# Performance work log

Measured on AMD Instinct MI355X. Metric: run time of the kernel, lower is better.

The kernel has to match this reference:

```python
import math
import jax, jax.numpy as jnp
import numpy as np

B, C, H, W = 32, 256, 32, 32  # in==mid==out channels

def setup_inputs() -> dict:
    key = jax.random.key(0)
    ks = jax.random.split(key, 3)
    x = jax.random.normal(ks[0], (B, C, H, W), dtype=jnp.float32)
    # 1x1 convs are just channel matmuls: weight [out_ch, in_ch]
    w_in = jax.random.normal(ks[1], (3 * C, C), dtype=jnp.float32) * (1.0 / math.sqrt(C))
    b_in = jnp.zeros((3 * C,), dtype=jnp.float32)
    # project_out has init_scale=0.0 in the original; we use random weights so the
    # output (and gradients) are non-trivial, but the math is identical.
    w_out = jax.random.normal(ks[2], (C, C), dtype=jnp.float32) * (1.0 / math.sqrt(C))
    b_out = jnp.zeros((C,), dtype=jnp.float32)
    return {"x": x, "w_in": w_in, "b_in": b_in, "w_out": w_out, "b_out": b_out}

def _qkv_attention(q, k, v):
    # q,k,v: [B,C,H,W]. Full spatial self-attention over the HxW grid.
    b, c, h, w = q.shape
    scores = jnp.einsum('bchw,bcHW->bhwHW', q, k)          # [B,H,W,H,W]
    scores = scores.reshape(b, h, w, h * w) / math.sqrt(c)
    attn = jax.nn.softmax(scores, axis=-1).reshape(b, h, w, h, w)
    return jnp.einsum('bhwHW,bcHW->bchw', attn, v)          # [B,C,H,W]

def reference(x, w_in, b_in, w_out, b_out):
    skip = x  # in_channels == out_channels -> Identity skip
    qkv = jnp.einsum('oc,bchw->bohw', w_in, x) + b_in[None, :, None, None]
    q, k, v = jnp.split(qkv, 3, axis=1)
    h = _qkv_attention(q, k, v)
    out = jnp.einsum('oc,bchw->bohw', w_out, h) + b_out[None, :, None, None]
    return out + skip
```

## Files before the change

### kernel.cpp

```cpp
#include <hip/hip_runtime.h>
#include <hip/hip_bf16.h>

typedef __attribute__((ext_vector_type(8))) short bf16x8;
typedef __attribute__((ext_vector_type(4))) float f32x4;
typedef __attribute__((ext_vector_type(16))) float f32x16;
typedef long long i64;

#define NB 32
#define NC 256
#define NN 1024

__device__ __forceinline__ unsigned pack2(float a, float b) {
    __hip_bfloat16 ha = __float2bfloat16(a), hb = __float2bfloat16(b);
    unsigned short ua = *(unsigned short*)&ha, ub = *(unsigned short*)&hb;
    return (unsigned)ua | ((unsigned)ub << 16);
}

__device__ __forceinline__ float bflo(unsigned u) {
    union { unsigned i; float f; } x; x.i = u << 16; return x.f;
}
__device__ __forceinline__ float bfhi(unsigned u) {
    union { unsigned i; float f; } x; x.i = u & 0xffff0000u; return x.f;
}
__device__ __forceinline__ unsigned fp8x4(float a, float b, float c, float d) {
    int w = __builtin_amdgcn_cvt_pk_fp8_f32(a, b, 0, false);
    w = __builtin_amdgcn_cvt_pk_fp8_f32(c, d, w, true);
    return (unsigned)w;
}

__device__ __forceinline__ void glds16(const void* g, void* lds) {
    __builtin_amdgcn_global_load_lds(
        (const __attribute__((address_space(1))) unsigned int*)g,
        (__attribute__((address_space(3))) unsigned int*)lds, 16, 0, 0);
}

__global__ __launch_bounds__(256) void xpose_kernel(
    const float* __restrict__ x, unsigned char* __restrict__ Xt8)
{
    __shared__ float Ls[64 * 67];
    const int t = threadIdx.x;
    const int n0 = blockIdx.x * 64, c0 = blockIdx.y * 64, b = blockIdx.z;
    const int cl = t >> 4, nl = (t & 15) * 4;
    const float* xb = x + ((size_t)b * NC + c0) * NN + n0;
    #pragma unroll
    for (int q4 = 0; q4 < 4; ++q4) {
        const int c = cl + q4 * 16;
        const float4 v = *(const float4*)(xb + (size_t)c * NN + nl);
        Ls[(nl + 0) * 67 + c] = v.x;
        Ls[(nl + 1) * 67 + c] = v.y;
        Ls[(nl + 2) * 67 + c] = v.z;
        Ls[(nl + 3) * 67 + c] = v.w;
    }
    __syncthreads();
    #pragma unroll
    for (int p = 0; p < 2; ++p) {
        const int idx = p * 256 + t, n = idx >> 3, cs = idx & 7;
        const float* r = &Ls[n * 67 + cs * 8];
        uint2 o;
        o.x = fp8x4(r[0], r[1], r[2], r[3]);
        o.y = fp8x4(r[4], r[5], r[6], r[7]);
        *(uint2*)(Xt8 + ((size_t)b * NN + n0 + n) * 256 + c0 + cs * 8) = o;
    }
}

__device__ __forceinline__ void stage_ab8(const unsigned char* __restrict__ Ag,
                                          const float* __restrict__ Bg,
                                          char* Ad, char* Bd, int ks, int t)
{
    #pragma unroll
    for (int p = 0; p < 2; ++p) {
        const int idx = p * 256 + t;
        const int row = idx >> 2, pc = idx & 3;
        const int lp = pc ^ (row & 3);
        glds16(Ag + (size_t)row * 256 + ks * 64 + lp * 16, Ad + idx * 16);
        const float* wp = Bg + (size_t)row * NC + ks * 64 + lp * 16;
        const float4 u0 = *(const float4*)wp;
        const float4 u1 = *(const float4*)(wp + 4);
        const float4 u2 = *(const float4*)(wp + 8);
        const float4 u3 = *(const float4*)(wp + 12);
        uint4 pk;
        pk.x = fp8x4(u0.x, u0.y, u0.z, u0.w);
        pk.y = fp8x4(u1.x, u1.y, u1.z, u1.w);
        pk.z = fp8x4(u2.x, u2.y, u2.z, u2.w);
        pk.w = fp8x4(u3.x, u3.y, u3.z, u3.w);
        *(uint4*)(Bd + idx * 16) = pk;
    }
}

__global__ __launch_bounds__(256, 3) void qkv_gemm_kernel(
    const unsigned char* __restrict__ Xt8, const float* __restrict__ w_in,
    const float* __restrict__ b_in, unsigned char* __restrict__ Qt8,
    unsigned char* __restrict__ Kt8, unsigned char* __restrict__ Vf8)
{
    __shared__ char smem[34816];
    char* const A0 = smem;
    char* const A1 = smem + 8192;
    char* const B0 = smem + 16384;
    char* const B1 = smem + 24576;

    const int t  = threadIdx.x;
    const int wv = t >> 6, ln = t & 63, lo = ln & 15, hi = ln >> 4;
    const int wm = wv >> 1, wn = wv & 1;
    const int n0 = blockIdx.x * 128, o0 = blockIdx.y * 128, b = blockIdx.z;

    const unsigned char* Ag = Xt8 + ((size_t)b * NN + n0) * 256;
    const float* Bg = w_in + (size_t)o0 * NC;

    f32x4 acc[4][4];
    #pragma unroll
    for (int i = 0; i < 4; ++i)
        #pragma unroll
        for (int j = 0; j < 4; ++j) acc[i][j] = (f32x4){0.f, 0.f, 0.f, 0.f};

    int ra[4], rb[4];
    #pragma unroll
    for (int f = 0; f < 4; ++f) { ra[f] = wm * 64 + f * 16 + lo; rb[f] = wn * 64 + f * 16 + lo; }

    stage_ab8(Ag, Bg, A0, B0, 0, t);
    __syncthreads();
    #pragma unroll
    for (int ks = 0; ks < 4; ++ks) {
        char* Ac = (ks & 1) ? A1 : A0;
        char* Bc = (ks & 1) ? B1 : B0;
        if (ks < 3)
            stage_ab8(Ag, Bg, (ks & 1) ? A0 : A1, (ks & 1) ? B0 : B1, ks + 1, t);
        #pragma unroll
        for (int kk = 0; kk < 2; ++kk) {
            i64 av[4], bv[4];
            #pragma unroll
            for (int f = 0; f < 4; ++f) {
                av[f] = *(const i64*)(Ac + ra[f] * 64 + (((kk << 2) | hi) ^ ((ra[f] & 3) << 1)) * 8);
                bv[f] = *(const i64*)(Bc + rb[f] * 64 + (((kk << 2) | hi) ^ ((rb[f] & 3) << 1)) * 8);
            }
            #pragma unroll
            for (int fm = 0; fm < 4; ++fm)
                #pragma unroll
                for (int fn = 0; fn < 4; ++fn)
                    acc[fm][fn] = __builtin_amdgcn_mfma_f32_16x16x32_fp8_fp8(
                        av[fm], bv[fn], acc[fm][fn], 0, 0, 0);
        }
        __syncthreads();
    }

    float bias[4];
    #pragma unroll
    for (int fn = 0; fn < 4; ++fn) bias[fn] = b_in[o0 + wn * 64 + fn * 16 + lo];

    __hip_bfloat16* Ls = (__hip_bfloat16*)smem;
    if (o0 < 512) {
        #pragma unroll
        for (int fm = 0; fm < 4; ++fm)
            #pragma unroll
            for (int fn = 0; fn < 4; ++fn)
                #pragma unroll
                for (int r = 0; r < 4; ++r)
                    Ls[(wm * 64 + fm * 16 + hi * 4 + r) * 136 + wn * 64 + fn * 16 + lo] =
                        __float2bfloat16(acc[fm][fn][r] + bias[fn]);
        __syncthreads();
        unsigned char* dst = (o0 < 256) ? Qt8 : Kt8;
        const int oc = (o0 < 256) ? o0 : o0 - 256;
        #pragma unroll
        for (int p = 0; p < 4; ++p) {
            const int idx = p * 256 + t, row = idx >> 3, ch = idx & 7;
            const unsigned* ls = (const unsigned*)&Ls[row * 136 + ch * 16];
            const uint4 a = *(const uint4*)ls;
            const uint4 b2 = *(const uint4*)(ls + 4);
            uint4 o;
            o.x = fp8x4(bflo(a.x), bfhi(a.x), bflo(a.y), bfhi(a.y));
            o.y = fp8x4(bflo(a.z), bfhi(a.z), bflo(a.w), bfhi(a.w));
            o.z = fp8x4(bflo(b2.x), bfhi(b2.x), bflo(b2.y), bfhi(b2.y));
            o.w = fp8x4(bflo(b2.z), bfhi(b2.z), bflo(b2.w), bfhi(b2.w));
            *(uint4*)(dst + ((size_t)b * NN + n0 + row) * 256 + oc + ch * 16) = o;
        }
    } else {
        #pragma unroll
        for (int fm = 0; fm < 4; ++fm)
            #pragma unroll
            for (int fn = 0; fn < 4; ++fn)
                #pragma unroll
                for (int r = 0; r < 4; ++r)
                    Ls[(wn * 64 + fn * 16 + lo) * 136 + wm * 64 + fm * 16 + hi * 4 + r] =
                        __float2bfloat16(acc[fm][fn][r] + bias[fn]);
        __syncthreads();
        #pragma unroll
        for (int p = 0; p < 8; ++p) {
            const int idx = p * 256 + t;
            const int ch = idx >> 7, cr = idx & 127;
            const unsigned* ls = (const unsigned*)&Ls[cr * 136 + ch * 8];
            const uint4 a = *(const uint4*)ls;
            uint2 o;
            o.x = fp8x4(bflo(a.x), bfhi(a.x), bflo(a.y), bfhi(a.y));
            o.y = fp8x4(bflo(a.z), bfhi(a.z), bflo(a.w), bfhi(a.w));
            const int g = (n0 >> 3) + ch;
            *(uint2*)(Vf8 + (((size_t)b * 128 + g) * 256 + (o0 - 512) + cr) * 8) = o;
        }
    }
}

__device__ __forceinline__ void stage_tile(const unsigned char* __restrict__ Kb,
                                           const unsigned char* __restrict__ Vb,
                                           char* Kd, char* Vd, int m0, int t)
{
    {
        const int row = t >> 4, pc = t & 15;
        const int prow = (row & 19) | ((row & 4) << 1) | ((row & 8) >> 1);
        const int sc = pc ^ (row & 15);
        glds16(Kb + (size_t)(m0 + prow) * 256 + sc * 16, Kd + t * 16);
    }
    {
        glds16(Vb + (size_t)(m0 >> 3) * 2048 + t * 16, Vd + t * 16);
    }
}

__global__ __launch_bounds__(512, 2) void attn_kernel(
    const unsigned char* __restrict__ Qt8, const unsigned char* __restrict__ Kt8,
    const unsigned char* __restrict__ Vf8, const float* __restrict__ w_out,
    const float* __restrict__ b_out, const float* __restrict__ xg,
    float* __restrict__ out)
{
    __shared__ char smem[139264];

    const int t  = threadIdx.x;
    const int wv = t >> 6, ln = t & 63;
    const int l32 = ln & 31, h2 = ln >> 5;
    const int qgrp = wv & 3, half = wv >> 2;
    const int wid = blockIdx.x + 8 * blockIdx.y;
    const int swz = (wid & 7) * 32 + (wid >> 3);
    const int qb = swz & 7, b = swz >> 3;
    const int n0 = qb * 128;
    const float scale = 0.0625f;

    const unsigned char* Kbase = Kt8 + (size_t)b * NN * 256;
    const unsigned char* Vbase = Vf8 + (size_t)b * 128 * 2048;

    const unsigned char* qp = Qt8 + ((size_t)b * NN + n0 + qgrp * 32 + l32) * 256;
    i64 qf[16];
    #pragma unroll
    for (int ks = 0; ks < 16; ++ks)
        qf[ks] = *(const i64*)(qp + ks * 16 + h2 * 8);

    f32x16 acc[8];
    #pragma unroll
    for (int ct = 0; ct < 8; ++ct)
        #pragma unroll
        for (int r = 0; r < 16; ++r) acc[ct][r] = 0.f;
    float mr = 0.f;
    float sr = 0.f;

    #pragma unroll
    for (int tt = 0; tt < 4; ++tt)
        stage_tile(Kbase, Vbase, smem + tt * 8192, smem + 32768 + tt * 8192,
                   tt * 32, t);
    __syncthreads();

    for (int s = 0; s < 16; ++s) {
        if (s < 15) {
            const int t2 = 2 * s + 2, t3 = 2 * s + 3;
            stage_tile(Kbase, Vbase, smem + (t2 & 3) * 8192,
                       smem + 32768 + (t2 & 3) * 8192, t2 * 32, t);
            stage_tile(Kbase, Vbase, smem + (t3 & 3) * 8192,
                       smem + 32768 + (t3 & 3) * 8192, t3 * 32, t);
        }
        const int tile = 2 * s + half;
        char* const Kc = smem + (tile & 3) * 8192;
        char* const Vc = smem + 32768 + (tile & 3) * 8192;

        f32x16 sfA, sfB;
        #pragma unroll
        for (int r = 0; r < 16; ++r) { sfA[r] = 0.f; sfB[r] = 0.f; }
        __builtin_amdgcn_s_setprio(1);
        #pragma unroll
        for (int ks = 0; ks < 8; ++ks) {
            const int pc = ks ^ (l32 & 15);
            const i64 kf = *(const i64*)(Kc + l32 * 256 + pc * 16 + h2 * 8);
            sfA = __builtin_amdgcn_mfma_f32_32x32x16_fp8_fp8(kf, qf[ks], sfA, 0, 0, 0);
        }
        #pragma unroll
        for (int ks = 8; ks < 16; ++ks) {
            const int pc = ks ^ (l32 & 15);
            const i64 kf = *(const i64*)(Kc + l32 * 256 + pc * 16 + h2 * 8);
            sfB = __builtin_amdgcn_mfma_f32_32x32x16_fp8_fp8(kf, qf[ks], sfB, 0, 0, 0);
        }
        __builtin_amdgcn_s_setprio(0);

        float sv[16];
        #pragma unroll
        for (int r = 0; r < 16; ++r) sv[r] = sfA[r] + sfB[r];

        float m0a = fmaxf(sv[0], sv[1]),  m1a = fmaxf(sv[2], sv[3]);
        float m2a = fmaxf(sv[4], sv[5]),  m3a = fmaxf(sv[6], sv[7]);
        float m4a = fmaxf(sv[8], sv[9]),  m5a = fmaxf(sv[10], sv[11]);
        float m6a = fmaxf(sv[12], sv[13]), m7a = fmaxf(sv[14], sv[15]);
        float m0b = fmaxf(m0a, m1a), m1b = fmaxf(m2a, m3a);
        float m2b = fmaxf(m4a, m5a), m3b = fmaxf(m6a, m7a);
        float tm = fmaxf(fmaxf(m0b, m1b), fmaxf(m2b, m3b));
        tm = fmaxf(tm, __shfl_xor(tm, 32, 64));
        tm *= scale;
        if (__any(tm > mr + 8.f)) {
            const float mn = fmaxf(mr, tm);
            const float al = __expf(mr - mn);
            mr = mn;
            sr *= al;
            #pragma unroll
            for (int ct = 0; ct < 8; ++ct)
                #pragma unroll
                for (int r = 0; r < 16; ++r) acc[ct][r] *= al;
        }
        float p[16];
        #pragma unroll
        for (int r = 0; r < 16; ++r)
            p[r] = __expf(sv[r] * scale - mr);
        float s0a = p[0] + p[1],  s1a = p[2] + p[3];
        float s2a = p[4] + p[5],  s3a = p[6] + p[7];
        float s4a = p[8] + p[9],  s5a = p[10] + p[11];
        float s6a = p[12] + p[13], s7a = p[14] + p[15];
        float sacc = ((s0a + s1a) + (s2a + s3a)) + ((s4a + s5a) + (s6a + s7a));
        sacc += __shfl_xor(sacc, 32, 64);
        sr += sacc;

        i64 pb[2];
        #pragma unroll
        for (int kstep = 0; kstep < 2; ++kstep) {
            union { unsigned u[2]; i64 l; } uu;
            uu.u[0] = fp8x4(p[8 * kstep + 0], p[8 * kstep + 1],
                            p[8 * kstep + 2], p[8 * kstep + 3]);
            uu.u[1] = fp8x4(p[8 * kstep + 4], p[8 * kstep + 5],
                            p[8 * kstep + 6], p[8 * kstep + 7]);
            pb[kstep] = uu.l;
        }

        __builtin_amdgcn_s_setprio(1);
        #pragma unroll
        for (int ct = 0; ct < 8; ++ct) {
            #pragma unroll
            for (int kstep = 0; kstep < 2; ++kstep) {
                const i64 vf = *(const i64*)(Vc + (2 * kstep + h2) * 2048 +
                                             (ct * 32 + l32) * 8);
                acc[ct] = __builtin_amdgcn_mfma_f32_32x32x16_fp8_fp8(vf, pb[kstep], acc[ct], 0, 0, 0);
            }
        }
        __builtin_amdgcn_s_setprio(0);
        __syncthreads();
    }

    const int wo = t >> 5, wck = t & 31;
    float4 wr[16];
    #pragma unroll
    for (int p = 0; p < 8; ++p) {
        const int o = p * 16 + wo;
        const float* wp = w_out + (size_t)o * NC + wck * 8;
        wr[2 * p]     = *(const float4*)wp;
        wr[2 * p + 1] = *(const float4*)(wp + 4);
    }

    float* const ex = (float*)smem;
    __hip_bfloat16* const Hld = (__hip_bfloat16*)(smem + 69632);
    #pragma unroll
    for (int ph = 0; ph < 2; ++ph) {
        if (half == 1 && (qgrp >> 1) == ph) {
            float* dst = ex + ((qgrp & 1) * 64 + ln) * 132;
            #pragma unroll
            for (int ct = 0; ct < 8; ++ct)
                #pragma unroll
                for (int rr = 0; rr < 4; ++rr) {
                    f32x4 v = {acc[ct][rr * 4 + 0], acc[ct][rr * 4 + 1],
                               acc[ct][rr * 4 + 2], acc[ct][rr * 4 + 3]};
                    *(f32x4*)(dst + ct * 16 + rr * 4) = v;
                }
            dst[128] = mr;
            dst[129] = sr;
        }
        __syncthreads();
        if (half == 0 && (qgrp >> 1) == ph) {
            const float* src = ex + ((qgrp & 1) * 64 + ln) * 132;
            const float mb = src[128], lb = src[129];
            const float m = fmaxf(mr, mb);
            float fa = __expf(mr - m), fb = __expf(mb - m);
            const float inv = 1.0f / (sr * fa + lb * fb);
            fa *= inv; fb *= inv;
            __hip_bfloat16* hrow = Hld + (size_t)(qgrp * 32 + l32) * 264;
            #pragma unroll
            for (int ct = 0; ct < 8; ++ct)
                #pragma unroll
                for (int ss = 0; ss < 4; ++ss) {
                    const float o0 = acc[ct][ss * 4 + 0] * fa + src[ct * 16 + ss * 4 + 0] * fb;
                    const float o1 = acc[ct][ss * 4 + 1] * fa + src[ct * 16 + ss * 4 + 1] * fb;
                    const float o2 = acc[ct][ss * 4 + 2] * fa + src[ct * 16 + ss * 4 + 2] * fb;
                    const float o3 = acc[ct][ss * 4 + 3] * fa + src[ct * 16 + ss * 4 + 3] * fb;
                    uint2 v;
                    v.x = pack2(o0, o1);
                    v.y = pack2(o2, o3);
                    *(uint2*)(hrow + ct * 32 + ss * 8 + h2 * 4) = v;
                }
        }
        __syncthreads();
    }

    __hip_bfloat16* const Wld = (__hip_bfloat16*)smem;
    const int oT = wv >> 1;
    const int nT0 = (wv & 1) * 2, nT1 = nT0 + 1;

    #pragma unroll
    for (int p = 0; p < 8; ++p) {
        const int o = p * 16 + wo;
        uint4 pk;
        pk.x = pack2(wr[2*p].x, wr[2*p].y);     pk.y = pack2(wr[2*p].z, wr[2*p].w);
        pk.z = pack2(wr[2*p+1].x, wr[2*p+1].y); pk.w = pack2(wr[2*p+1].z, wr[2*p+1].w);
        *(uint4*)((char*)Wld + (size_t)o * 528 + wck * 16) = pk;
    }
    #pragma unroll
    for (int p = 0; p < 8; ++p) {
        const int o = 128 + p * 16 + wo;
        const float* wp = w_out + (size_t)o * NC + wck * 8;
        wr[2 * p]     = *(const float4*)wp;
        wr[2 * p + 1] = *(const float4*)(wp + 4);
    }
    __syncthreads();

    #pragma unroll
    for (int oh = 0; oh < 2; ++oh) {
        f32x16 oc0, oc1;
        #pragma unroll
        for (int r = 0; r < 16; ++r) { oc0[r] = 0.f; oc1[r] = 0.f; }
        __builtin_amdgcn_s_setprio(1);
        #pragma unroll
        for (int ks = 0; ks < 16; ++ks) {
            const int ck = ks * 2 + h2;
            bf16x8 wf = *(const bf16x8*)((char*)Wld + (size_t)(oT * 32 + l32) * 528 + ck * 16);
            bf16x8 hf0 = *(const bf16x8*)((char*)Hld + (size_t)(nT0 * 32 + l32) * 528 + ck * 16);
            bf16x8 hf1 = *(const bf16x8*)((char*)Hld + (size_t)(nT1 * 32 + l32) * 528 + ck * 16);
            oc0 = __builtin_amdgcn_mfma_f32_32x32x16_bf16(wf, hf0, oc0, 0, 0, 0);
            oc1 = __builtin_amdgcn_mfma_f32_32x32x16_bf16(wf, hf1, oc1, 0, 0, 0);
        }
        __builtin_amdgcn_s_setprio(0);

        #pragma unroll
        for (int r = 0; r < 16; ++r) {
            const int o = oh * 128 + oT * 32 + (r & 3) + 8 * (r >> 2) + 4 * h2;
            const float bo = b_out[o];
            const size_t rowg = ((size_t)b * NC + o) * NN + n0;
            const size_t g0 = rowg + nT0 * 32 + l32;
            const size_t g1 = rowg + nT1 * 32 + l32;
            out[g0] = oc0[r] + bo + xg[g0];
            out[g1] = oc1[r] + bo + xg[g1];
        }
        __syncthreads();
        if (oh == 0) {
            #pragma unroll
            for (int p = 0; p < 8; ++p) {
                const int o = p * 16 + wo;
                uint4 pk;
                pk.x = pack2(wr[2*p].x, wr[2*p].y);     pk.y = pack2(wr[2*p].z, wr[2*p].w);
                pk.z = pack2(wr[2*p+1].x, wr[2*p+1].y); pk.w = pack2(wr[2*p+1].z, wr[2*p+1].w);
                *(uint4*)((char*)Wld + (size_t)o * 528 + wck * 16) = pk;
            }
            __syncthreads();
        }
    }
}

extern "C" void kernel_launch(void* const* d_in, const int* in_sizes, int n_in,
                              void* d_out, int out_size, void* d_ws, size_t ws_size,
                              hipStream_t stream) {
    const float* x     = (const float*)d_in[0];
    const float* w_in  = (const float*)d_in[1];
    const float* b_in  = (const float*)d_in[2];
    const float* w_out = (const float*)d_in[3];
    const float* b_out = (const float*)d_in[4];
    float* out = (float*)d_out;

    if (ws_size < (size_t)64 * 1024 * 1024) return;
    char* ws = (char*)d_ws;
    unsigned char* Qt8 = (unsigned char*)(ws);
    unsigned char* Kt8 = (unsigned char*)(ws + ((size_t)8 << 20));
    unsigned char* Vf8 = (unsigned char*)(ws + ((size_t)16 << 20));
    unsigned char* Xt8 = (unsigned char*)(ws + ((size_t)24 << 20));

    xpose_kernel<<<dim3(16, 4, 32), 256, 0, stream>>>(x, Xt8);
    qkv_gemm_kernel<<<dim3(8, 6, 32), 256, 0, stream>>>(Xt8, w_in, b_in, Qt8, Kt8, Vf8);
    attn_kernel<<<dim3(8, 32), 512, 0, stream>>>(Qt8, Kt8, Vf8, w_out, b_out, x, out);
}
```

Before: 84.37 us.

## Fuse input transpose and FP8 cast into the QKV GEMM, two output tiles per block

Drops the separate transpose kernel and the Xt8 intermediate. The QKV GEMM now streams fp32 x tiles straight into LDS with global_load_lds and builds the fp8 A-fragments in registers. Each block computes two output-channel tiles, so the x tile it loads serves both. This saves one launch and a global round-trip of x, but adds LDS gathers and fp8 conversion inside the GEMM loop, more accumulator registers, and lower occupancy (launch bound 2, larger LDS).

```diff
diff --git a/kernel.cpp b/kernel.cpp
--- a/kernel.cpp
+++ b/kernel.cpp
@@ -34,167 +34,163 @@
         (__attribute__((address_space(3))) unsigned int*)lds, 16, 0, 0);
 }
 
-__global__ __launch_bounds__(256) void xpose_kernel(
-    const float* __restrict__ x, unsigned char* __restrict__ Xt8)
-{
-    __shared__ float Ls[64 * 67];
-    const int t = threadIdx.x;
-    const int n0 = blockIdx.x * 64, c0 = blockIdx.y * 64, b = blockIdx.z;
-    const int cl = t >> 4, nl = (t & 15) * 4;
-    const float* xb = x + ((size_t)b * NC + c0) * NN + n0;
-    #pragma unroll
-    for (int q4 = 0; q4 < 4; ++q4) {
-        const int c = cl + q4 * 16;
-        const float4 v = *(const float4*)(xb + (size_t)c * NN + nl);
-        Ls[(nl + 0) * 67 + c] = v.x;
-        Ls[(nl + 1) * 67 + c] = v.y;
-        Ls[(nl + 2) * 67 + c] = v.z;
-        Ls[(nl + 3) * 67 + c] = v.w;
-    }
-    __syncthreads();
-    #pragma unroll
-    for (int p = 0; p < 2; ++p) {
-        const int idx = p * 256 + t, n = idx >> 3, cs = idx & 7;
-        const float* r = &Ls[n * 67 + cs * 8];
-        uint2 o;
-        o.x = fp8x4(r[0], r[1], r[2], r[3]);
-        o.y = fp8x4(r[4], r[5], r[6], r[7]);
-        *(uint2*)(Xt8 + ((size_t)b * NN + n0 + n) * 256 + c0 + cs * 8) = o;
-    }
-}
-
-__device__ __forceinline__ void stage_ab8(const unsigned char* __restrict__ Ag,
-                                          const float* __restrict__ Bg,
-                                          char* Ad, char* Bd, int ks, int t)
-{
-    #pragma unroll
-    for (int p = 0; p < 2; ++p) {
-        const int idx = p * 256 + t;
-        const int row = idx >> 2, pc = idx & 3;
-        const int lp = pc ^ (row & 3);
-        glds16(Ag + (size_t)row * 256 + ks * 64 + lp * 16, Ad + idx * 16);
-        const float* wp = Bg + (size_t)row * NC + ks * 64 + lp * 16;
-        const float4 u0 = *(const float4*)wp;
-        const float4 u1 = *(const float4*)(wp + 4);
-        const float4 u2 = *(const float4*)(wp + 8);
-        const float4 u3 = *(const float4*)(wp + 12);
-        uint4 pk;
-        pk.x = fp8x4(u0.x, u0.y, u0.z, u0.w);
-        pk.y = fp8x4(u1.x, u1.y, u1.z, u1.w);
-        pk.z = fp8x4(u2.x, u2.y, u2.z, u2.w);
-        pk.w = fp8x4(u3.x, u3.y, u3.z, u3.w);
-        *(uint4*)(Bd + idx * 16) = pk;
-    }
-}
-
-__global__ __launch_bounds__(256, 3) void qkv_gemm_kernel(
-    const unsigned char* __restrict__ Xt8, const float* __restrict__ w_in,
+__global__ __launch_bounds__(256, 2) void qkv_fused_kernel(
+    const float* __restrict__ x, const float* __restrict__ w_in,
     const float* __restrict__ b_in, unsigned char* __restrict__ Qt8,
     unsigned char* __restrict__ Kt8, unsigned char* __restrict__ Vf8)
 {
-    __shared__ char smem[34816];
-    char* const A0 = smem;
-    char* const A1 = smem + 8192;
-    char* const B0 = smem + 16384;
-    char* const B1 = smem + 24576;
-
+    __shared__ char smem[49664];
     const int t  = threadIdx.x;
     const int wv = t >> 6, ln = t & 63, lo = ln & 15, hi = ln >> 4;
     const int wm = wv >> 1, wn = wv & 1;
-    const int n0 = blockIdx.x * 128, o0 = blockIdx.y * 128, b = blockIdx.z;
-
-    const unsigned char* Ag = Xt8 + ((size_t)b * NN + n0) * 256;
-    const float* Bg = w_in + (size_t)o0 * NC;
-
-    f32x4 acc[4][4];
-    #pragma unroll
-    for (int i = 0; i < 4; ++i)
-        #pragma unroll
-        for (int j = 0; j < 4; ++j) acc[i][j] = (f32x4){0.f, 0.f, 0.f, 0.f};
+    const int n0 = blockIdx.x * 128, y = blockIdx.y, b = blockIdx.z;
+    const int ot0 = y, ot1 = y + 3;
+
+    const float* xb = x + (size_t)b * NC * NN;
+
+    f32x4 acc[2][4][4];
+    #pragma unroll
+    for (int g = 0; g < 2; ++g)
+        #pragma unroll
+        for (int i = 0; i < 4; ++i)
+            #pragma unroll
+            for (int j = 0; j < 4; ++j) acc[g][i][j] = (f32x4){0.f, 0.f, 0.f, 0.f};
 
     int ra[4], rb[4];
     #pragma unroll
     for (int f = 0; f < 4; ++f) { ra[f] = wm * 64 + f * 16 + lo; rb[f] = wn * 64 + f * 16 + lo; }
 
-    stage_ab8(Ag, Bg, A0, B0, 0, t);
+    #define XBUF(bf) (smem + (bf) * 16640)
+    #define BBUF(bf, og) (smem + 33280 + (bf) * 8192 + (og) * 4096)
+    auto stage = [&](int ks, int bf) {
+        #pragma unroll
+        for (int p = 0; p < 4; ++p) {
+            const int idx = p * 256 + t;
+            const int pair = idx >> 6, sub = idx & 63;
+            const int c = ks * 32 + pair * 2 + (sub >> 5);
+            glds16(xb + (size_t)c * NN + n0 + (sub & 31) * 4, XBUF(bf) + pair * 1040);
+        }
+        #pragma unroll
+        for (int og = 0; og < 2; ++og) {
+            const int o = t >> 1, m = t & 1;
+            const int otile = og ? ot1 : ot0;
+            const float* wp = w_in + (size_t)(otile * 128 + o) * NC + ks * 32 + m * 16;
+            const float4 u0 = *(const float4*)wp;
+            const float4 u1 = *(const float4*)(wp + 4);
+            const float4 u2 = *(const float4*)(wp + 8);
+            const float4 u3 = *(const float4*)(wp + 12);
+            uint4 pk;
+            pk.x = fp8x4(u0.x, u0.y, u0.z, u0.w);
+            pk.y = fp8x4(u1.x, u1.y, u1.z, u1.w);
+            pk.z = fp8x4(u2.x, u2.y, u2.z, u2.w);
+            pk.w = fp8x4(u3.x, u3.y, u3.z, u3.w);
+            const int slot = m ^ ((o >> 2) & 1);
+            *(uint4*)(BBUF(bf, og) + o * 32 + slot * 16) = pk;
+        }
+    };
+
+    stage(0, 0);
     __syncthreads();
-    #pragma unroll
-    for (int ks = 0; ks < 4; ++ks) {
-        char* Ac = (ks & 1) ? A1 : A0;
-        char* Bc = (ks & 1) ? B1 : B0;
-        if (ks < 3)
-            stage_ab8(Ag, Bg, (ks & 1) ? A0 : A1, (ks & 1) ? B0 : B1, ks + 1, t);
-        #pragma unroll
-        for (int kk = 0; kk < 2; ++kk) {
-            i64 av[4], bv[4];
+    for (int ks = 0; ks < 8; ++ks) {
+        const int cur = ks & 1;
+        if (ks < 7) stage(ks + 1, cur ^ 1);
+
+        const float* Xc = (const float*)XBUF(cur);
+        i64 av[4];
+        #pragma unroll
+        for (int f = 0; f < 4; ++f) {
+            const int n = ra[f];
+            float v[8];
+            #pragma unroll
+            for (int j = 0; j < 8; ++j) {
+                const int c = hi * 8 + j;
+                v[j] = Xc[c * 128 + (c >> 1) * 4 + n];
+            }
+            union { unsigned u[2]; i64 l; } uu;
+            uu.u[0] = fp8x4(v[0], v[1], v[2], v[3]);
+            uu.u[1] = fp8x4(v[4], v[5], v[6], v[7]);
+            av[f] = uu.l;
+        }
+        #pragma unroll
+        for (int og = 0; og < 2; ++og) {
+            i64 bv[4];
             #pragma unroll
             for (int f = 0; f < 4; ++f) {
-                av[f] = *(const i64*)(Ac + ra[f] * 64 + (((kk << 2) | hi) ^ ((ra[f] & 3) << 1)) * 8);
-                bv[f] = *(const i64*)(Bc + rb[f] * 64 + (((kk << 2) | hi) ^ ((rb[f] & 3) << 1)) * 8);
+                const int o = rb[f];
+                const int phys8 = hi ^ (((o >> 2) & 1) << 1);
+                bv[f] = *(const i64*)(BBUF(cur, og) + o * 32 + phys8 * 8);
             }
             #pragma unroll
             for (int fm = 0; fm < 4; ++fm)
                 #pragma unroll
                 for (int fn = 0; fn < 4; ++fn)
-                    acc[fm][fn] = __builtin_amdgcn_mfma_f32_16x16x32_fp8_fp8(
-                        av[fm], bv[fn], acc[fm][fn], 0, 0, 0);
-        }
-        __syncthreads();
-    }
-
-    float bias[4];
-    #pragma unroll
-    for (int fn = 0; fn < 4; ++fn) bias[fn] = b_in[o0 + wn * 64 + fn * 16 + lo];
+                    acc[og][fm][fn] = __builtin_amdgcn_mfma_f32_16x16x32_fp8_fp8(
+                        av[fm], bv[fn], acc[og][fm][fn], 0, 0, 0);
+        }
+        __syncthreads();
+    }
 
     __hip_bfloat16* Ls = (__hip_bfloat16*)smem;
-    if (o0 < 512) {
-        #pragma unroll
-        for (int fm = 0; fm < 4; ++fm)
-            #pragma unroll
-            for (int fn = 0; fn < 4; ++fn)
-                #pragma unroll
-                for (int r = 0; r < 4; ++r)
-                    Ls[(wm * 64 + fm * 16 + hi * 4 + r) * 136 + wn * 64 + fn * 16 + lo] =
-                        __float2bfloat16(acc[fm][fn][r] + bias[fn]);
-        __syncthreads();
-        unsigned char* dst = (o0 < 256) ? Qt8 : Kt8;
-        const int oc = (o0 < 256) ? o0 : o0 - 256;
-        #pragma unroll
-        for (int p = 0; p < 4; ++p) {
-            const int idx = p * 256 + t, row = idx >> 3, ch = idx & 7;
-            const unsigned* ls = (const unsigned*)&Ls[row * 136 + ch * 16];
-            const uint4 a = *(const uint4*)ls;
-            const uint4 b2 = *(const uint4*)(ls + 4);
-            uint4 o;
-            o.x = fp8x4(bflo(a.x), bfhi(a.x), bflo(a.y), bfhi(a.y));
-            o.y = fp8x4(bflo(a.z), bfhi(a.z), bflo(a.w), bfhi(a.w));
-            o.z = fp8x4(bflo(b2.x), bfhi(b2.x), bflo(b2.y), bfhi(b2.y));
-            o.w = fp8x4(bflo(b2.z), bfhi(b2.z), bflo(b2.w), bfhi(b2.w));
-            *(uint4*)(dst + ((size_t)b * NN + n0 + row) * 256 + oc + ch * 16) = o;
-        }
-    } else {
-        #pragma unroll
-        for (int fm = 0; fm < 4; ++fm)
-            #pragma unroll
-            for (int fn = 0; fn < 4; ++fn)
-                #pragma unroll
-                for (int r = 0; r < 4; ++r)
-                    Ls[(wn * 64 + fn * 16 + lo) * 136 + wm * 64 + fm * 16 + hi * 4 + r] =
-                        __float2bfloat16(acc[fm][fn][r] + bias[fn]);
-        __syncthreads();
-        #pragma unroll
-        for (int p = 0; p < 8; ++p) {
-            const int idx = p * 256 + t;
-            const int ch = idx >> 7, cr = idx & 127;
-            const unsigned* ls = (const unsigned*)&Ls[cr * 136 + ch * 8];
-            const uint4 a = *(const uint4*)ls;
-            uint2 o;
-            o.x = fp8x4(bflo(a.x), bfhi(a.x), bflo(a.y), bfhi(a.y));
-            o.y = fp8x4(bflo(a.z), bfhi(a.z), bflo(a.w), bfhi(a.w));
-            const int g = (n0 >> 3) + ch;
-            *(uint2*)(Vf8 + (((size_t)b * 128 + g) * 256 + (o0 - 512) + cr) * 8) = o;
-        }
-    }
+    #pragma unroll
+    for (int og = 0; og < 2; ++og) {
+        const int otile = og ? ot1 : ot0;
+        const int o0 = otile * 128;
+        float bias[4];
+        #pragma unroll
+        for (int fn = 0; fn < 4; ++fn) bias[fn] = b_in[o0 + wn * 64 + fn * 16 + lo];
+
+        if (o0 < 512) {
+            #pragma unroll
+            for (int fm = 0; fm < 4; ++fm)
+                #pragma unroll
+                for (int fn = 0; fn < 4; ++fn)
+                    #pragma unroll
+                    for (int r = 0; r < 4; ++r)
+                        Ls[(wm * 64 + fm * 16 + hi * 4 + r) * 136 + wn * 64 + fn * 16 + lo] =
+                            __float2bfloat16(acc[og][fm][fn][r] + bias[fn]);
+            __syncthreads();
+            unsigned char* dst = (o0 < 256) ? Qt8 : Kt8;
+            const int oc = (o0 < 256) ? o0 : o0 - 256;
+            #pragma unroll
+            for (int p = 0; p < 4; ++p) {
+                const int idx = p * 256 + t, row = idx >> 3, ch = idx & 7;
+                const unsigned* ls = (const unsigned*)&Ls[row * 136 + ch * 16];
+                const uint4 a = *(const uint4*)ls;
+                const uint4 b2 = *(const uint4*)(ls + 4);
+                uint4 o;
+                o.x = fp8x4(bflo(a.x), bfhi(a.x), bflo(a.y), bfhi(a.y));
+                o.y = fp8x4(bflo(a.z), bfhi(a.z), bflo(a.w), bfhi(a.w));
+                o.z = fp8x4(bflo(b2.x), bfhi(b2.x), bflo(b2.y), bfhi(b2.y));
+                o.w = fp8x4(bflo(b2.z), bfhi(b2.z), bflo(b2.w), bfhi(b2.w));
+                *(uint4*)(dst + ((size_t)b * NN + n0 + row) * 256 + oc + ch * 16) = o;
+            }
+        } else {
+            #pragma unroll
+            for (int fm = 0; fm < 4; ++fm)
+                #pragma unroll
+                for (int fn = 0; fn < 4; ++fn)
+                    #pragma unroll
+                    for (int r = 0; r < 4; ++r)
+                        Ls[(wn * 64 + fn * 16 + lo) * 136 + wm * 64 + fm * 16 + hi * 4 + r] =
+                            __float2bfloat16(acc[og][fm][fn][r] + bias[fn]);
+            __syncthreads();
+            #pragma unroll
+            for (int p = 0; p < 8; ++p) {
+                const int idx = p * 256 + t;
+                const int ch = idx >> 7, cr = idx & 127;
+                const unsigned* ls = (const unsigned*)&Ls[cr * 136 + ch * 8];
+                const uint4 a = *(const uint4*)ls;
+                uint2 o;
+                o.x = fp8x4(bflo(a.x), bfhi(a.x), bflo(a.y), bfhi(a.y));
+                o.y = fp8x4(bflo(a.z), bfhi(a.z), bflo(a.w), bfhi(a.w));
+                const int g = (n0 >> 3) + ch;
+                *(uint2*)(Vf8 + (((size_t)b * 128 + g) * 256 + (o0 - 512) + cr) * 8) = o;
+            }
+        }
+        __syncthreads();
+    }
+    #undef XBUF
+    #undef BBUF
 }
 
 __device__ __forceinline__ void stage_tile(const unsigned char* __restrict__ Kb,
@@ -469,14 +465,12 @@
     const float* b_out = (const float*)d_in[4];
     float* out = (float*)d_out;
 
-    if (ws_size < (size_t)64 * 1024 * 1024) return;
+    if (ws_size < (size_t)24 * 1024 * 1024) return;
     char* ws = (char*)d_ws;
     unsigned char* Qt8 = (unsigned char*)(ws);
     unsigned char* Kt8 = (unsigned char*)(ws + ((size_t)8 << 20));
     unsigned char* Vf8 = (unsigned char*)(ws + ((size_t)16 << 20));
-    unsigned char* Xt8 = (unsigned char*)(ws + ((size_t)24 << 20));
-
-    xpose_kernel<<<dim3(16, 4, 32), 256, 0, stream>>>(x, Xt8);
-    qkv_gemm_kernel<<<dim3(8, 6, 32), 256, 0, stream>>>(Xt8, w_in, b_in, Qt8, Kt8, Vf8);
+
+    qkv_fused_kernel<<<dim3(8, 3, 32), 256, 0, stream>>>(x, w_in, b_in, Qt8, Kt8, Vf8);
     attn_kernel<<<dim3(8, 32), 512, 0, stream>>>(Qt8, Kt8, Vf8, w_out, b_out, x, out);
 }
```

Result: slower. 87.39 us (+3.6%).

## Software-pipeline PV MFMAs one tile behind QK MFMAs in attention loop

Applied to the files above, without the earlier changes.

Defers each tile's P·V MFMA accumulation to the next loop iteration, where it is issued right after the current tile's QK^T MFMAs. The aim is to overlap the softmax/exp work with matrix work and shorten the per-iteration dependency chain. To keep the deferred V tile alive, V staging grows from 4 to 8 LDS slots, and a tail PV step runs after the loop. The w_out prefetch into registers is replaced by a direct load-convert-store per output half, which lowers register pressure but adds a global load before each projection half.

```diff
diff --git a/kernel.cpp b/kernel.cpp
--- a/kernel.cpp
+++ b/kernel.cpp
@@ -249,21 +249,25 @@
 
     #pragma unroll
     for (int tt = 0; tt < 4; ++tt)
-        stage_tile(Kbase, Vbase, smem + tt * 8192, smem + 32768 + tt * 8192,
-                   tt * 32, t);
+        stage_tile(Kbase, Vbase, smem + (tt & 3) * 8192,
+                   smem + 32768 + (tt & 7) * 8192, tt * 32, t);
     __syncthreads();
+
+    i64 pb_prev[2];
+    pb_prev[0] = 0; pb_prev[1] = 0;
+    const char* Vc_prev = smem + 32768;
 
     for (int s = 0; s < 16; ++s) {
         if (s < 15) {
             const int t2 = 2 * s + 2, t3 = 2 * s + 3;
             stage_tile(Kbase, Vbase, smem + (t2 & 3) * 8192,
-                       smem + 32768 + (t2 & 3) * 8192, t2 * 32, t);
+                       smem + 32768 + (t2 & 7) * 8192, t2 * 32, t);
             stage_tile(Kbase, Vbase, smem + (t3 & 3) * 8192,
-                       smem + 32768 + (t3 & 3) * 8192, t3 * 32, t);
+                       smem + 32768 + (t3 & 7) * 8192, t3 * 32, t);
         }
         const int tile = 2 * s + half;
         char* const Kc = smem + (tile & 3) * 8192;
-        char* const Vc = smem + 32768 + (tile & 3) * 8192;
+        char* const Vc = smem + 32768 + (tile & 7) * 8192;
 
         f32x16 sfA, sfB;
         #pragma unroll
@@ -280,6 +284,18 @@
             const int pc = ks ^ (l32 & 15);
             const i64 kf = *(const i64*)(Kc + l32 * 256 + pc * 16 + h2 * 8);
             sfB = __builtin_amdgcn_mfma_f32_32x32x16_fp8_fp8(kf, qf[ks], sfB, 0, 0, 0);
+        }
+
+        if (s > 0) {
+            #pragma unroll
+            for (int ct = 0; ct < 8; ++ct) {
+                #pragma unroll
+                for (int kstep = 0; kstep < 2; ++kstep) {
+                    const i64 vf = *(const i64*)(Vc_prev + (2 * kstep + h2) * 2048 +
+                                                 (ct * 32 + l32) * 8);
+                    acc[ct] = __builtin_amdgcn_mfma_f32_32x32x16_fp8_fp8(vf, pb_prev[kstep], acc[ct], 0, 0, 0);
+                }
+            }
         }
         __builtin_amdgcn_s_setprio(0);
 
@@ -318,7 +334,6 @@
         sacc += __shfl_xor(sacc, 32, 64);
         sr += sacc;
 
-        i64 pb[2];
         #pragma unroll
         for (int kstep = 0; kstep < 2; ++kstep) {
             union { unsigned u[2]; i64 l; } uu;
@@ -326,32 +341,23 @@
                             p[8 * kstep + 2], p[8 * kstep + 3]);
             uu.u[1] = fp8x4(p[8 * kstep + 4], p[8 * kstep + 5],
                             p[8 * kstep + 6], p[8 * kstep + 7]);
-            pb[kstep] = uu.l;
-        }
-
-        __builtin_amdgcn_s_setprio(1);
-        #pragma unroll
-        for (int ct = 0; ct < 8; ++ct) {
-            #pragma unroll
-            for (int kstep = 0; kstep < 2; ++kstep) {
-                const i64 vf = *(const i64*)(Vc + (2 * kstep + h2) * 2048 +
-                                             (ct * 32 + l32) * 8);
-                acc[ct] = __builtin_amdgcn_mfma_f32_32x32x16_fp8_fp8(vf, pb[kstep], acc[ct], 0, 0, 0);
-            }
-        }
-        __builtin_amdgcn_s_setprio(0);
-        __syncthreads();
-    }
-
-    const int wo = t >> 5, wck = t & 31;
-    float4 wr[16];
-    #pragma unroll
-    for (int p = 0; p < 8; ++p) {
-        const int o = p * 16 + wo;
-        const float* wp = w_out + (size_t)o * NC + wck * 8;
-        wr[2 * p]     = *(const float4*)wp;
-        wr[2 * p + 1] = *(const float4*)(wp + 4);
-    }
+            pb_prev[kstep] = uu.l;
+        }
+        Vc_prev = Vc;
+        __syncthreads();
+    }
+
+    __builtin_amdgcn_s_setprio(1);
+    #pragma unroll
+    for (int ct = 0; ct < 8; ++ct) {
+        #pragma unroll
+        for (int kstep = 0; kstep < 2; ++kstep) {
+            const i64 vf = *(const i64*)(Vc_prev + (2 * kstep + h2) * 2048 +
+                                         (ct * 32 + l32) * 8);
+            acc[ct] = __builtin_amdgcn_mfma_f32_32x32x16_fp8_fp8(vf, pb_prev[kstep], acc[ct], 0, 0, 0);
+        }
+    }
+    __builtin_amdgcn_s_setprio(0);
 
     float* const ex = (float*)smem;
     __hip_bfloat16* const Hld = (__hip_bfloat16*)(smem + 69632);
@@ -399,26 +405,21 @@
     __hip_bfloat16* const Wld = (__hip_bfloat16*)smem;
     const int oT = wv >> 1;
     const int nT0 = (wv & 1) * 2, nT1 = nT0 + 1;
-
-    #pragma unroll
-    for (int p = 0; p < 8; ++p) {
-        const int o = p * 16 + wo;
-        uint4 pk;
-        pk.x = pack2(wr[2*p].x, wr[2*p].y);     pk.y = pack2(wr[2*p].z, wr[2*p].w);
-        pk.z = pack2(wr[2*p+1].x, wr[2*p+1].y); pk.w = pack2(wr[2*p+1].z, wr[2*p+1].w);
-        *(uint4*)((char*)Wld + (size_t)o * 528 + wck * 16) = pk;
-    }
-    #pragma unroll
-    for (int p = 0; p < 8; ++p) {
-        const int o = 128 + p * 16 + wo;
-        const float* wp = w_out + (size_t)o * NC + wck * 8;
-        wr[2 * p]     = *(const float4*)wp;
-        wr[2 * p + 1] = *(const float4*)(wp + 4);
-    }
-    __syncthreads();
-
-    #pragma unroll
     for (int oh = 0; oh < 2; ++oh) {
+        #pragma unroll
+        for (int p = 0; p < 8; ++p) {
+            const int idx = p * 512 + t;
+            const int o = idx >> 5, ck = idx & 31;
+            const float* wp = w_out + (size_t)(oh * 128 + o) * NC + ck * 8;
+            const float4 u0 = *(const float4*)wp;
+            const float4 u1 = *(const float4*)(wp + 4);
+            uint4 pk;
+            pk.x = pack2(u0.x, u0.y); pk.y = pack2(u0.z, u0.w);
+            pk.z = pack2(u1.x, u1.y); pk.w = pack2(u1.z, u1.w);
+            *(uint4*)((char*)Wld + (size_t)o * 528 + ck * 16) = pk;
+        }
+        __syncthreads();
+
         f32x16 oc0, oc1;
         #pragma unroll
         for (int r = 0; r < 16; ++r) { oc0[r] = 0.f; oc1[r] = 0.f; }
@@ -445,17 +446,6 @@
             out[g1] = oc1[r] + bo + xg[g1];
         }
         __syncthreads();
-        if (oh == 0) {
-            #pragma unroll
-            for (int p = 0; p < 8; ++p) {
-                const int o = p * 16 + wo;
-                uint4 pk;
-                pk.x = pack2(wr[2*p].x, wr[2*p].y);     pk.y = pack2(wr[2*p].z, wr[2*p].w);
-                pk.z = pack2(wr[2*p+1].x, wr[2*p+1].y); pk.w = pack2(wr[2*p+1].z, wr[2*p+1].w);
-                *(uint4*)((char*)Wld + (size_t)o * 528 + wck * 16) = pk;
-            }
-            __syncthreads();
-        }
     }
 }
 
@@ -469,7 +459,7 @@
     const float* b_out = (const float*)d_in[4];
     float* out = (float*)d_out;
 
-    if (ws_size < (size_t)64 * 1024 * 1024) return;
+    if (ws_size < (size_t)32 * 1024 * 1024) return;
     char* ws = (char*)d_ws;
     unsigned char* Qt8 = (unsigned char*)(ws);
     unsigned char* Kt8 = (unsigned char*)(ws + ((size_t)8 << 20));
```

Measured after the change: 85.86 us. No clear change (+1.8%).
